# Kernel optimization log

Measured on AMD Instinct MI355X. Metric: run time of the kernel, lower is better.

Reference implementation:

```python
import jax, jax.numpy as jnp
import numpy as np

B, C, H = 8, 512, 2048
GROUPS = 32
EPS = 1e-6


def setup_inputs() -> dict:
    key = jax.random.key(0)
    ks = jax.random.split(key, 10)
    s = 1.0 / np.sqrt(C)
    return {
        "x": jax.random.normal(ks[0], (B, C, H), dtype=jnp.float32),
        "gamma": jnp.ones((C,), jnp.float32),
        "beta": jnp.zeros((C,), jnp.float32),
        "wq": jax.random.normal(ks[1], (C, C), jnp.float32) * s,
        "bq": jnp.zeros((C,), jnp.float32),
        "wk": jax.random.normal(ks[2], (C, C), jnp.float32) * s,
        "bk": jnp.zeros((C,), jnp.float32),
        "wv": jax.random.normal(ks[3], (C, C), jnp.float32) * s,
        "bv": jnp.zeros((C,), jnp.float32),
        "wp": jax.random.normal(ks[4], (C, C), jnp.float32) * s,
        "bp": jnp.zeros((C,), jnp.float32),
    }


def group_norm(x, gamma, beta):
    b, c, h = x.shape
    xr = x.reshape(b, GROUPS, c // GROUPS, h)
    mean = xr.mean(axis=(2, 3), keepdims=True)
    var = xr.var(axis=(2, 3), keepdims=True)
    xn = ((xr - mean) * jax.lax.rsqrt(var + EPS)).reshape(b, c, h)
    return xn * gamma[None, :, None] + beta[None, :, None]


def conv1x1(x, w, b):
    # 1x1 Conv1d == channel-mixing GEMM: [C_out,C_in] x [b,C_in,h]
    return jnp.einsum("oc,bch->boh", w, x) + b[None, :, None]


def reference(x, gamma, beta, wq, bq, wk, bk, wv, bv, wp, bp):
    b, c, h = x.shape
    hn = group_norm(x, gamma, beta)
    q = conv1x1(hn, wq, bq)  # [b,c,h]
    k = conv1x1(hn, wk, bk)
    v = conv1x1(hn, wv, bv)
    # scores w[b,i,j] = sum_c q[b,c,i] k[b,c,j] / sqrt(c)
    w = jnp.einsum("bci,bcj->bij", q, k) * (c ** -0.5)
    w = jax.nn.softmax(w, axis=2)
    # h_[b,c,i] = sum_j v[b,c,j] w[b,i,j]
    h_ = jnp.einsum("bcj,bij->bci", v, w)
    out = conv1x1(h_, wp, bp)
    return x + out
```

## Files before the change

### kernel.cpp

```cpp
#include <hip/hip_runtime.h>
#include <stdint.h>

typedef unsigned short u16;
typedef short s16x8 __attribute__((ext_vector_type(8)));
typedef float f32x4 __attribute__((ext_vector_type(4)));

#define BM 128
#define BN 128
#define BK 32
#define KPAD 40

__device__ __forceinline__ float bf2f(u16 b) {
    union { unsigned int u; float f; } v; v.u = ((unsigned int)b) << 16; return v.f;
}
__device__ __forceinline__ u16 f2bf(float f) {
    union { float f; unsigned int u; } v; v.f = f;
    unsigned int u = v.u;
    u += 0x7fffu + ((u >> 16) & 1u);
    return (u16)(u >> 16);
}
__device__ __forceinline__ void async_cp16(const u16* g, u16* l) {
    __builtin_amdgcn_global_load_lds((const __attribute__((address_space(1))) void*)g,
                                     (__attribute__((address_space(3))) void*)l, 16, 0, 0);
}

__global__ __launch_bounds__(256) void gn_stats(const float* __restrict__ x,
                                                float* __restrict__ mean,
                                                float* __restrict__ rstd) {
    const int bg = blockIdx.x;
    const float* p = x + (long)bg * 16 * 2048;
    float s = 0.f, ss = 0.f;
    for (int it = 0; it < 32; it++) {
        const float4 v = *reinterpret_cast<const float4*>(p + ((it * 256 + threadIdx.x) << 2));
        s += v.x + v.y + v.z + v.w;
        ss += v.x * v.x + v.y * v.y + v.z * v.z + v.w * v.w;
    }
    const int lane = threadIdx.x & 63, wave = threadIdx.x >> 6;
#pragma unroll
    for (int o = 32; o > 0; o >>= 1) { s += __shfl_down(s, o, 64); ss += __shfl_down(ss, o, 64); }
    __shared__ float rb[8];
    if (lane == 0) { rb[wave] = s; rb[4 + wave] = ss; }
    __syncthreads();
    if (threadIdx.x == 0) {
        float S = rb[0] + rb[1] + rb[2] + rb[3];
        float SS = rb[4] + rb[5] + rb[6] + rb[7];
        float mu = S * (1.f / 32768.f);
        float var = SS * (1.f / 32768.f) - mu * mu;
        mean[bg] = mu;
        rstd[bg] = rsqrtf(var + 1e-6f);
    }
}

__global__ __launch_bounds__(256) void gn_apply_t(const float* __restrict__ x,
                                                  const float* __restrict__ gamma,
                                                  const float* __restrict__ beta,
                                                  const float* __restrict__ mean,
                                                  const float* __restrict__ rstd,
                                                  u16* __restrict__ hnT) {
    const int b = blockIdx.z, c0 = blockIdx.y * 64, h0 = blockIdx.x * 64;
    __shared__ __align__(16) u16 T[64][72];
    const int tid = threadIdx.x;
#pragma unroll
    for (int sidx = 0; sidx < 4; sidx++) {
        int ch = tid + sidx * 256;
        int cc = ch >> 4, h4 = (ch & 15) * 4;
        int c = c0 + cc;
        float mu = mean[b * 32 + (c >> 4)], rs = rstd[b * 32 + (c >> 4)];
        float ga = gamma[c], be = beta[c];
        const float4 v = *reinterpret_cast<const float4*>(x + ((long)b * 512 + c) * 2048 + h0 + h4);
        ushort4 pk;
        pk.x = f2bf((v.x - mu) * rs * ga + be);
        pk.y = f2bf((v.y - mu) * rs * ga + be);
        pk.z = f2bf((v.z - mu) * rs * ga + be);
        pk.w = f2bf((v.w - mu) * rs * ga + be);
        *reinterpret_cast<ushort4*>(&T[cc][h4]) = pk;
    }
    __syncthreads();
#pragma unroll
    for (int sidx = 0; sidx < 2; sidx++) {
        int ch = tid + sidx * 256;
        int hh = ch >> 3, c8 = (ch & 7) * 8;
        unsigned int o[4];
#pragma unroll
        for (int i = 0; i < 4; i++) {
            u16 lo = T[c8 + 2 * i][hh];
            u16 hi = T[c8 + 2 * i + 1][hh];
            o[i] = (unsigned int)lo | ((unsigned int)hi << 16);
        }
        *reinterpret_cast<uint4*>(hnT + ((long)b * 2048 + h0 + hh) * 512 + c0 + c8) =
            uint4{o[0], o[1], o[2], o[3]};
    }
}

__global__ __launch_bounds__(256) void w2bf(const float* __restrict__ a,
                                            const float* __restrict__ b,
                                            const float* __restrict__ c,
                                            u16* __restrict__ dst) {
    const float* s = (blockIdx.y == 0) ? a : (blockIdx.y == 1) ? b : c;
    const int i = (blockIdx.x * 256 + threadIdx.x) * 4;
    const float4 v = *reinterpret_cast<const float4*>(s + i);
    ushort4 p;
    p.x = f2bf(v.x); p.y = f2bf(v.y); p.z = f2bf(v.z); p.w = f2bf(v.w);
    *reinterpret_cast<ushort4*>(dst + (long)blockIdx.y * 262144 + i) = p;
}

__global__ __launch_bounds__(256) void softmax_rows(u16* __restrict__ S) {
    u16* p = S + (long)blockIdx.x * 2048;
    const int tid = threadIdx.x;
    uint4 v = *reinterpret_cast<const uint4*>(p + (tid << 3));
    unsigned int w[4] = {v.x, v.y, v.z, v.w};
    float f[8];
#pragma unroll
    for (int i = 0; i < 4; i++) {
        f[2 * i]     = bf2f((u16)(w[i] & 0xffffu));
        f[2 * i + 1] = bf2f((u16)(w[i] >> 16));
    }
    float m = f[0];
#pragma unroll
    for (int i = 1; i < 8; i++) m = fmaxf(m, f[i]);
    const int lane = tid & 63, wave = tid >> 6;
#pragma unroll
    for (int o = 32; o > 0; o >>= 1) m = fmaxf(m, __shfl_down(m, o, 64));
    __shared__ float rb[4];
    __shared__ float bc;
    if (lane == 0) rb[wave] = m;
    __syncthreads();
    if (tid == 0) bc = fmaxf(fmaxf(rb[0], rb[1]), fmaxf(rb[2], rb[3]));
    __syncthreads();
    m = bc;
    float s = 0.f;
#pragma unroll
    for (int i = 0; i < 8; i++) { f[i] = __expf(f[i] - m); s += f[i]; }
#pragma unroll
    for (int o = 32; o > 0; o >>= 1) s += __shfl_down(s, o, 64);
    __syncthreads();
    if (lane == 0) rb[wave] = s;
    __syncthreads();
    if (tid == 0) bc = 1.f / (rb[0] + rb[1] + rb[2] + rb[3]);
    __syncthreads();
    const float inv = bc;
#pragma unroll
    for (int i = 0; i < 4; i++)
        w[i] = (unsigned int)f2bf(f[2 * i] * inv) | ((unsigned int)f2bf(f[2 * i + 1] * inv) << 16);
    *reinterpret_cast<uint4*>(p + (tid << 3)) = uint4{w[0], w[1], w[2], w[3]};
}

template <int EPI>
__global__ __launch_bounds__(256) void gemm_tn_a(const u16* __restrict__ Ag, long sA,
                                                 const u16* __restrict__ Bg, long sB,
                                                 const float* __restrict__ bias,
                                                 const float* __restrict__ Xg, long sX,
                                                 void* __restrict__ Ogv, long sO,
                                                 int K, int lda, int ldb, int ldo,
                                                 float scale) {
    const int b = blockIdx.z;
    Ag += (long)b * sA;
    Bg += (long)b * sB;
    const int m0 = blockIdx.y * BM;
    const int n0 = blockIdx.x * BN;

    __shared__ __align__(16) u16 As[BM * BK];
    __shared__ __align__(16) u16 Bs[BN * BK];

    const int tid = threadIdx.x;
    const int wave = tid >> 6;
    const int lane = tid & 63;
    const int quad = lane >> 4;
    const int l16 = lane & 15;
    const int wm = (wave >> 1) * 64;
    const int wn = (wave & 1) * 64;
    const int rl = lane >> 2;
    const int cl = (lane & 3) * 8;

    f32x4 acc[4][4];
#pragma unroll
    for (int i = 0; i < 4; i++)
#pragma unroll
        for (int j = 0; j < 4; j++) acc[i][j] = f32x4{0.f, 0.f, 0.f, 0.f};

    for (int k0 = 0; k0 < K; k0 += BK) {
        __syncthreads();
#pragma unroll
        for (int j = 0; j < 2; j++) {
            const int rbase = wave * 32 + j * 16;
            async_cp16(Ag + (long)(m0 + rbase + rl) * lda + k0 + cl, &As[rbase * BK]);
            async_cp16(Bg + (long)(n0 + rbase + rl) * ldb + k0 + cl, &Bs[rbase * BK]);
        }
        __syncthreads();
        s16x8 af[4], bfr[4];
#pragma unroll
        for (int i = 0; i < 4; i++)
            af[i] = *reinterpret_cast<const s16x8*>(&As[(wm + i * 16 + l16) * BK + quad * 8]);
#pragma unroll
        for (int j = 0; j < 4; j++)
            bfr[j] = *reinterpret_cast<const s16x8*>(&Bs[(wn + j * 16 + l16) * BK + quad * 8]);
#pragma unroll
        for (int i = 0; i < 4; i++)
#pragma unroll
            for (int j = 0; j < 4; j++)
                acc[i][j] = __builtin_amdgcn_mfma_f32_16x16x32_bf16(af[i], bfr[j], acc[i][j], 0, 0, 0);
    }

#pragma unroll
    for (int i = 0; i < 4; i++) {
        const int mb = m0 + wm + i * 16 + quad * 4;
#pragma unroll
        for (int j = 0; j < 4; j++) {
            const int n = n0 + wn + j * 16 + l16;
            if (EPI == 0) {
                u16* O = (u16*)Ogv + (long)b * sO;
#pragma unroll
                for (int r = 0; r < 4; r++) {
                    float vv = acc[i][j][r] * scale;
                    if (bias) vv += bias[mb + r];
                    O[(long)(mb + r) * ldo + n] = f2bf(vv);
                }
            } else if (EPI == 1) {
                u16* O = (u16*)Ogv + (long)b * sO;
                ushort4 pk;
                pk.x = f2bf(acc[i][j][0] + bias[mb + 0]);
                pk.y = f2bf(acc[i][j][1] + bias[mb + 1]);
                pk.z = f2bf(acc[i][j][2] + bias[mb + 2]);
                pk.w = f2bf(acc[i][j][3] + bias[mb + 3]);
                *reinterpret_cast<ushort4*>(&O[(long)n * ldo + mb]) = pk;
            } else {
                float* O = (float*)Ogv + (long)b * sO;
                const float* X = Xg + (long)b * sX;
                const float bn = bias[n];
                const float4 xv = *reinterpret_cast<const float4*>(&X[(long)n * ldo + mb]);
                float4 pk;
                pk.x = acc[i][j][0] + bn + xv.x;
                pk.y = acc[i][j][1] + bn + xv.y;
                pk.z = acc[i][j][2] + bn + xv.z;
                pk.w = acc[i][j][3] + bn + xv.w;
                *reinterpret_cast<float4*>(&O[(long)n * ldo + mb]) = pk;
            }
        }
    }
}

template <int F32>
__device__ __forceinline__ void stage_tile(const char* G, int ld, int r0, int k0,
                                           u16* __restrict__ lds, int tid) {
    if (F32) {
        const float* g = (const float*)G;
#pragma unroll
        for (int s = 0; s < 4; s++) {
            const int c = tid + s * 256;
            const int row = c >> 3, col = (c & 7) * 4;
            const float4 v = *reinterpret_cast<const float4*>(g + (long)(r0 + row) * ld + k0 + col);
            ushort4 pk;
            pk.x = f2bf(v.x); pk.y = f2bf(v.y); pk.z = f2bf(v.z); pk.w = f2bf(v.w);
            *reinterpret_cast<ushort4*>(&lds[row * KPAD + col]) = pk;
        }
    } else {
        const u16* g = (const u16*)G;
#pragma unroll
        for (int s = 0; s < 2; s++) {
            const int c = tid + s * 256;
            const int row = c >> 2, col = (c & 3) * 8;
            const uint4 v = *reinterpret_cast<const uint4*>(g + (long)(r0 + row) * ld + k0 + col);
            *reinterpret_cast<uint4*>(&lds[row * KPAD + col]) = v;
        }
    }
}

template <int EPI, int AF32, int BF32>
__global__ __launch_bounds__(256) void gemm_tn(const void* __restrict__ Agv, long sA,
                                               const void* __restrict__ Bgv, long sB,
                                               const float* __restrict__ bias,
                                               const float* __restrict__ Xg, long sX,
                                               void* __restrict__ Ogv, long sO,
                                               int K, int lda, int ldb, int ldo,
                                               float scale) {
    const int b = blockIdx.z;
    const char* A8 = (const char*)Agv + (long)b * sA * (AF32 ? 4 : 2);
    const char* B8 = (const char*)Bgv + (long)b * sB * (BF32 ? 4 : 2);
    const int m0 = blockIdx.y * BM;
    const int n0 = blockIdx.x * BN;

    __shared__ __align__(16) u16 As[BM * KPAD];
    __shared__ __align__(16) u16 Bs[BN * KPAD];

    const int tid = threadIdx.x;
    const int wave = tid >> 6;
    const int lane = tid & 63;
    const int quad = lane >> 4;
    const int l16 = lane & 15;
    const int wm = (wave >> 1) * 64;
    const int wn = (wave & 1) * 64;

    f32x4 acc[4][4];
#pragma unroll
    for (int i = 0; i < 4; i++)
#pragma unroll
        for (int j = 0; j < 4; j++) acc[i][j] = f32x4{0.f, 0.f, 0.f, 0.f};

    for (int k0 = 0; k0 < K; k0 += BK) {
        __syncthreads();
        stage_tile<AF32>(A8, lda, m0, k0, As, tid);
        stage_tile<BF32>(B8, ldb, n0, k0, Bs, tid);
        __syncthreads();
        s16x8 af[4], bfr[4];
#pragma unroll
        for (int i = 0; i < 4; i++)
            af[i] = *reinterpret_cast<const s16x8*>(&As[(wm + i * 16 + l16) * KPAD + quad * 8]);
#pragma unroll
        for (int j = 0; j < 4; j++)
            bfr[j] = *reinterpret_cast<const s16x8*>(&Bs[(wn + j * 16 + l16) * KPAD + quad * 8]);
#pragma unroll
        for (int i = 0; i < 4; i++)
#pragma unroll
            for (int j = 0; j < 4; j++)
                acc[i][j] = __builtin_amdgcn_mfma_f32_16x16x32_bf16(af[i], bfr[j], acc[i][j], 0, 0, 0);
    }

#pragma unroll
    for (int i = 0; i < 4; i++) {
        const int mb = m0 + wm + i * 16 + quad * 4;
#pragma unroll
        for (int j = 0; j < 4; j++) {
            const int n = n0 + wn + j * 16 + l16;
            if (EPI == 0) {
                u16* O = (u16*)Ogv + (long)b * sO;
#pragma unroll
                for (int r = 0; r < 4; r++) {
                    float vv = acc[i][j][r] * scale;
                    if (bias) vv += bias[mb + r];
                    O[(long)(mb + r) * ldo + n] = f2bf(vv);
                }
            } else if (EPI == 1) {
                u16* O = (u16*)Ogv + (long)b * sO;
                ushort4 pk;
                pk.x = f2bf(acc[i][j][0] + bias[mb + 0]);
                pk.y = f2bf(acc[i][j][1] + bias[mb + 1]);
                pk.z = f2bf(acc[i][j][2] + bias[mb + 2]);
                pk.w = f2bf(acc[i][j][3] + bias[mb + 3]);
                *reinterpret_cast<ushort4*>(&O[(long)n * ldo + mb]) = pk;
            } else {
                float* O = (float*)Ogv + (long)b * sO;
                const float* X = Xg + (long)b * sX;
                const float bn = bias[n];
                const float4 xv = *reinterpret_cast<const float4*>(&X[(long)n * ldo + mb]);
                float4 pk;
                pk.x = acc[i][j][0] + bn + xv.x;
                pk.y = acc[i][j][1] + bn + xv.y;
                pk.z = acc[i][j][2] + bn + xv.z;
                pk.w = acc[i][j][3] + bn + xv.w;
                *reinterpret_cast<float4*>(&O[(long)n * ldo + mb]) = pk;
            }
        }
    }
}

extern "C" void kernel_launch(void* const* d_in, const int* in_sizes, int n_in,
                              void* d_out, int out_size, void* d_ws, size_t ws_size,
                              hipStream_t stream) {
    const float* x     = (const float*)d_in[0];
    const float* gamma = (const float*)d_in[1];
    const float* beta  = (const float*)d_in[2];
    const float* wq    = (const float*)d_in[3];
    const float* bq    = (const float*)d_in[4];
    const float* wk    = (const float*)d_in[5];
    const float* bk    = (const float*)d_in[6];
    const float* wv    = (const float*)d_in[7];
    const float* bv    = (const float*)d_in[8];
    const float* wp    = (const float*)d_in[9];
    const float* bp    = (const float*)d_in[10];
    float* out = (float*)d_out;

    const long HC = (long)2048 * 512;
    const long HH = (long)2048 * 2048;
    const long WSZ = 512 * 512;
    const float scl = 0.044194173824159216f;

    char* ws = (char*)d_ws;
    float* meanb = (float*)ws;
    float* rstdb = (float*)(ws + 1024);
    u16* base = (u16*)(ws + 4096);

    const size_t FULL_NEED   = 4096 + 2 * (size_t)(24 * HC + 8 * HH);
    const size_t MED_NEED    = 4096 + 2 * (size_t)(32 * HC + HH);
    const size_t SMALL_NEED  = 4096 + 2 * (size_t)(4 * HC + HH);
    const size_t CHUNK512    = 4096 + 2 * (size_t)(4 * HC + 512 * 2048);

    gn_stats<<<256, 256, 0, stream>>>(x, meanb, rstdb);

    if (ws_size >= FULL_NEED) {
        u16* qT  = base;
        u16* kT  = qT + 8 * HC;
        u16* vv  = kT + 8 * HC;
        u16* Sb  = vv + 8 * HC;
        u16* hnT = Sb;
        u16* wb3 = Sb + 8 * HH - 3 * WSZ;
        u16* hT  = qT;
        u16* wpb = vv;

        w2bf<<<dim3(256, 3), 256, 0, stream>>>(wq, wk, wv, wb3);
        gn_apply_t<<<dim3(32, 8, 8), 256, 0, stream>>>(x, gamma, beta, meanb, rstdb, hnT);
        gemm_tn_a<1><<<dim3(16, 4, 8), 256, 0, stream>>>(wb3 + 0 * WSZ, 0, hnT, HC, bq, nullptr, 0,
                                                         qT, HC, 512, 512, 512, 512, 1.f);
        gemm_tn_a<1><<<dim3(16, 4, 8), 256, 0, stream>>>(wb3 + 1 * WSZ, 0, hnT, HC, bk, nullptr, 0,
                                                         kT, HC, 512, 512, 512, 512, 1.f);
        gemm_tn_a<0><<<dim3(16, 4, 8), 256, 0, stream>>>(wb3 + 2 * WSZ, 0, hnT, HC, bv, nullptr, 0,
                                                         vv, HC, 512, 512, 512, 2048, 1.f);
        gemm_tn_a<0><<<dim3(16, 16, 8), 256, 0, stream>>>(qT, HC, kT, HC, nullptr, nullptr, 0,
                                                          Sb, HH, 512, 512, 512, 2048, scl);
        softmax_rows<<<16384, 256, 0, stream>>>(Sb);
        gemm_tn_a<0><<<dim3(4, 16, 8), 256, 0, stream>>>(Sb, HH, vv, HC, nullptr, nullptr, 0,
                                                         hT, HC, 2048, 2048, 2048, 512, 1.f);
        w2bf<<<dim3(256, 1), 256, 0, stream>>>(wp, wp, wp, wpb);
        gemm_tn_a<2><<<dim3(4, 16, 8), 256, 0, stream>>>(hT, HC, wpb, 0, bp, x, HC,
                                                         out, HC, 512, 512, 512, 2048, 1.f);
    } else if (ws_size >= MED_NEED) {
        u16* hnT = base;
        u16* qT  = hnT + 8 * HC;
        u16* kT  = qT + 8 * HC;
        u16* vv  = kT + 8 * HC;
        u16* Sb  = vv + 8 * HC;
        u16* hT  = hnT;
        gn_apply_t<<<dim3(32, 8, 8), 256, 0, stream>>>(x, gamma, beta, meanb, rstdb, hnT);
        gemm_tn<1, 1, 0><<<dim3(16, 4, 8), 256, 0, stream>>>(wq, 0, hnT, HC, bq, nullptr, 0,
                                                             qT, HC, 512, 512, 512, 512, 1.f);
        gemm_tn<1, 1, 0><<<dim3(16, 4, 8), 256, 0, stream>>>(wk, 0, hnT, HC, bk, nullptr, 0,
                                                             kT, HC, 512, 512, 512, 512, 1.f);
        gemm_tn<0, 1, 0><<<dim3(16, 4, 8), 256, 0, stream>>>(wv, 0, hnT, HC, bv, nullptr, 0,
                                                             vv, HC, 512, 512, 512, 2048, 1.f);
        for (int b = 0; b < 8; b++) {
            gemm_tn<0, 0, 0><<<dim3(16, 16, 1), 256, 0, stream>>>(qT + b * HC, 0, kT + b * HC, 0,
                                                                  nullptr, nullptr, 0, Sb, 0,
                                                                  512, 512, 512, 2048, scl);
            softmax_rows<<<2048, 256, 0, stream>>>(Sb);
            gemm_tn<0, 0, 0><<<dim3(4, 16, 1), 256, 0, stream>>>(Sb, 0, vv + b * HC, 0,
                                                                 nullptr, nullptr, 0, hT + b * HC, 0,
                                                                 2048, 2048, 2048, 512, 1.f);
        }
        gemm_tn<2, 0, 1><<<dim3(4, 16, 8), 256, 0, stream>>>(hT, HC, wp, 0, bp, x, HC,
                                                             out, HC, 512, 512, 512, 2048, 1.f);
    } else {
        const int CH = (ws_size >= SMALL_NEED) ? 2048 : ((ws_size >= CHUNK512) ? 512 : 128);
        u16* hn = base;
        u16* q  = hn + HC;
        u16* k  = q + HC;
        u16* v  = k + HC;
        u16* Sc = v + HC;
        u16* hT = hn;
        for (int b = 0; b < 8; b++) {
            const float* xb = x + (long)b * HC;
            gn_apply_t<<<dim3(32, 8, 1), 256, 0, stream>>>(xb, gamma, beta,
                                                           meanb + b * 32, rstdb + b * 32, hn);
            gemm_tn<1, 1, 0><<<dim3(16, 4, 1), 256, 0, stream>>>(wq, 0, hn, 0, bq, nullptr, 0,
                                                                 q, 0, 512, 512, 512, 512, 1.f);
            gemm_tn<1, 1, 0><<<dim3(16, 4, 1), 256, 0, stream>>>(wk, 0, hn, 0, bk, nullptr, 0,
                                                                 k, 0, 512, 512, 512, 512, 1.f);
            gemm_tn<0, 1, 0><<<dim3(16, 4, 1), 256, 0, stream>>>(wv, 0, hn, 0, bv, nullptr, 0,
                                                                 v, 0, 512, 512, 512, 2048, 1.f);
            for (int i0 = 0; i0 < 2048; i0 += CH) {
                gemm_tn<0, 0, 0><<<dim3(16, CH / 128, 1), 256, 0, stream>>>(
                    q + (long)i0 * 512, 0, k, 0, nullptr, nullptr, 0, Sc, 0,
                    512, 512, 512, 2048, scl);
                softmax_rows<<<CH, 256, 0, stream>>>(Sc);
                gemm_tn<0, 0, 0><<<dim3(4, CH / 128, 1), 256, 0, stream>>>(
                    Sc, 0, v, 0, nullptr, nullptr, 0, hT + (long)i0 * 512, 0,
                    2048, 2048, 2048, 512, 1.f);
            }
            gemm_tn<2, 0, 1><<<dim3(4, 16, 1), 256, 0, stream>>>(hT, 0, wp, 0, bp, xb, 0,
                                                                 out + (long)b * HC, 0,
                                                                 512, 512, 512, 2048, 1.f);
        }
    }
}
```

Before: 337.2 us.

## Double-buffer LDS staging in GEMM and fuse QKV projections into one launch

The GEMM main loop now keeps two LDS buffers and issues the async global-to-LDS copy for the next K tile before computing on the current one. This hides load latency and cuts the barriers per K step from two to one. The three separate Q/K/V projection launches are merged into one kernel with a grid of 24 in z, which picks weight, bias and output layout per block. This removes two launches and gives a larger grid, at the cost of doubled LDS per block, which may reduce occupancy.

```diff
diff --git a/kernel.cpp b/kernel.cpp
--- a/kernel.cpp
+++ b/kernel.cpp
@@ -159,8 +159,8 @@
     const int m0 = blockIdx.y * BM;
     const int n0 = blockIdx.x * BN;
 
-    __shared__ __align__(16) u16 As[BM * BK];
-    __shared__ __align__(16) u16 Bs[BN * BK];
+    __shared__ __align__(16) u16 As[2][BM * BK];
+    __shared__ __align__(16) u16 Bs[2][BN * BK];
 
     const int tid = threadIdx.x;
     const int wave = tid >> 6;
@@ -178,27 +178,37 @@
 #pragma unroll
         for (int j = 0; j < 4; j++) acc[i][j] = f32x4{0.f, 0.f, 0.f, 0.f};
 
-    for (int k0 = 0; k0 < K; k0 += BK) {
-        __syncthreads();
+    auto stage = [&](int buf, int k0) {
 #pragma unroll
         for (int j = 0; j < 2; j++) {
             const int rbase = wave * 32 + j * 16;
-            async_cp16(Ag + (long)(m0 + rbase + rl) * lda + k0 + cl, &As[rbase * BK]);
-            async_cp16(Bg + (long)(n0 + rbase + rl) * ldb + k0 + cl, &Bs[rbase * BK]);
-        }
-        __syncthreads();
+            async_cp16(Ag + (long)(m0 + rbase + rl) * lda + k0 + cl, &As[buf][rbase * BK]);
+            async_cp16(Bg + (long)(n0 + rbase + rl) * ldb + k0 + cl, &Bs[buf][rbase * BK]);
+        }
+    };
+    auto compute = [&](int buf) {
         s16x8 af[4], bfr[4];
 #pragma unroll
         for (int i = 0; i < 4; i++)
-            af[i] = *reinterpret_cast<const s16x8*>(&As[(wm + i * 16 + l16) * BK + quad * 8]);
+            af[i] = *reinterpret_cast<const s16x8*>(&As[buf][(wm + i * 16 + l16) * BK + quad * 8]);
 #pragma unroll
         for (int j = 0; j < 4; j++)
-            bfr[j] = *reinterpret_cast<const s16x8*>(&Bs[(wn + j * 16 + l16) * BK + quad * 8]);
+            bfr[j] = *reinterpret_cast<const s16x8*>(&Bs[buf][(wn + j * 16 + l16) * BK + quad * 8]);
 #pragma unroll
         for (int i = 0; i < 4; i++)
 #pragma unroll
             for (int j = 0; j < 4; j++)
                 acc[i][j] = __builtin_amdgcn_mfma_f32_16x16x32_bf16(af[i], bfr[j], acc[i][j], 0, 0, 0);
+    };
+
+    stage(0, 0);
+    for (int k0 = 0; k0 < K; k0 += 2 * BK) {
+        __syncthreads();
+        stage(1, k0 + BK);
+        compute(0);
+        __syncthreads();
+        if (k0 + 2 * BK < K) stage(0, k0 + 2 * BK);
+        compute(1);
     }
 
 #pragma unroll
@@ -239,6 +249,106 @@
     }
 }
 
+__global__ __launch_bounds__(256) void qkv_a(const u16* __restrict__ wb3,
+                                             const u16* __restrict__ hnT,
+                                             const float* __restrict__ bq,
+                                             const float* __restrict__ bk,
+                                             const float* __restrict__ bv,
+                                             u16* __restrict__ qT, u16* __restrict__ kT,
+                                             u16* __restrict__ vv) {
+    const long HC = 1048576;
+    const int z = blockIdx.z;
+    const int which = z % 3, b = z / 3;
+    const u16* Ag = wb3 + which * 262144;
+    const u16* Bg = hnT + (long)b * HC;
+    const int m0 = blockIdx.y * BM;
+    const int n0 = blockIdx.x * BN;
+
+    __shared__ __align__(16) u16 As[2][BM * BK];
+    __shared__ __align__(16) u16 Bs[2][BN * BK];
+
+    const int tid = threadIdx.x;
+    const int wave = tid >> 6;
+    const int lane = tid & 63;
+    const int quad = lane >> 4;
+    const int l16 = lane & 15;
+    const int wm = (wave >> 1) * 64;
+    const int wn = (wave & 1) * 64;
+    const int rl = lane >> 2;
+    const int cl = (lane & 3) * 8;
+
+    f32x4 acc[4][4];
+#pragma unroll
+    for (int i = 0; i < 4; i++)
+#pragma unroll
+        for (int j = 0; j < 4; j++) acc[i][j] = f32x4{0.f, 0.f, 0.f, 0.f};
+
+    auto stage = [&](int buf, int k0) {
+#pragma unroll
+        for (int j = 0; j < 2; j++) {
+            const int rbase = wave * 32 + j * 16;
+            async_cp16(Ag + (long)(m0 + rbase + rl) * 512 + k0 + cl, &As[buf][rbase * BK]);
+            async_cp16(Bg + (long)(n0 + rbase + rl) * 512 + k0 + cl, &Bs[buf][rbase * BK]);
+        }
+    };
+    auto compute = [&](int buf) {
+        s16x8 af[4], bfr[4];
+#pragma unroll
+        for (int i = 0; i < 4; i++)
+            af[i] = *reinterpret_cast<const s16x8*>(&As[buf][(wm + i * 16 + l16) * BK + quad * 8]);
+#pragma unroll
+        for (int j = 0; j < 4; j++)
+            bfr[j] = *reinterpret_cast<const s16x8*>(&Bs[buf][(wn + j * 16 + l16) * BK + quad * 8]);
+#pragma unroll
+        for (int i = 0; i < 4; i++)
+#pragma unroll
+            for (int j = 0; j < 4; j++)
+                acc[i][j] = __builtin_amdgcn_mfma_f32_16x16x32_bf16(af[i], bfr[j], acc[i][j], 0, 0, 0);
+    };
+
+    stage(0, 0);
+    for (int k0 = 0; k0 < 512; k0 += 2 * BK) {
+        __syncthreads();
+        stage(1, k0 + BK);
+        compute(0);
+        __syncthreads();
+        if (k0 + 2 * BK < 512) stage(0, k0 + 2 * BK);
+        compute(1);
+    }
+
+    if (which == 2) {
+        u16* O = vv + (long)b * HC;
+#pragma unroll
+        for (int i = 0; i < 4; i++) {
+            const int mb = m0 + wm + i * 16 + quad * 4;
+#pragma unroll
+            for (int j = 0; j < 4; j++) {
+                const int n = n0 + wn + j * 16 + l16;
+#pragma unroll
+                for (int r = 0; r < 4; r++)
+                    O[(long)(mb + r) * 2048 + n] = f2bf(acc[i][j][r] + bv[mb + r]);
+            }
+        }
+    } else {
+        const float* bias = which ? bk : bq;
+        u16* O = (which ? kT : qT) + (long)b * HC;
+#pragma unroll
+        for (int i = 0; i < 4; i++) {
+            const int mb = m0 + wm + i * 16 + quad * 4;
+#pragma unroll
+            for (int j = 0; j < 4; j++) {
+                const int n = n0 + wn + j * 16 + l16;
+                ushort4 pk;
+                pk.x = f2bf(acc[i][j][0] + bias[mb + 0]);
+                pk.y = f2bf(acc[i][j][1] + bias[mb + 1]);
+                pk.z = f2bf(acc[i][j][2] + bias[mb + 2]);
+                pk.w = f2bf(acc[i][j][3] + bias[mb + 3]);
+                *reinterpret_cast<ushort4*>(&O[(long)n * 512 + mb]) = pk;
+            }
+        }
+    }
+}
+
 template <int F32>
 __device__ __forceinline__ void stage_tile(const char* G, int ld, int r0, int k0,
                                            u16* __restrict__ lds, int tid) {
@@ -398,12 +508,7 @@
 
         w2bf<<<dim3(256, 3), 256, 0, stream>>>(wq, wk, wv, wb3);
         gn_apply_t<<<dim3(32, 8, 8), 256, 0, stream>>>(x, gamma, beta, meanb, rstdb, hnT);
-        gemm_tn_a<1><<<dim3(16, 4, 8), 256, 0, stream>>>(wb3 + 0 * WSZ, 0, hnT, HC, bq, nullptr, 0,
-                                                         qT, HC, 512, 512, 512, 512, 1.f);
-        gemm_tn_a<1><<<dim3(16, 4, 8), 256, 0, stream>>>(wb3 + 1 * WSZ, 0, hnT, HC, bk, nullptr, 0,
-                                                         kT, HC, 512, 512, 512, 512, 1.f);
-        gemm_tn_a<0><<<dim3(16, 4, 8), 256, 0, stream>>>(wb3 + 2 * WSZ, 0, hnT, HC, bv, nullptr, 0,
-                                                         vv, HC, 512, 512, 512, 2048, 1.f);
+        qkv_a<<<dim3(16, 4, 24), 256, 0, stream>>>(wb3, hnT, bq, bk, bv, qT, kT, vv);
         gemm_tn_a<0><<<dim3(16, 16, 8), 256, 0, stream>>>(qT, HC, kT, HC, nullptr, nullptr, 0,
                                                           Sb, HH, 512, 512, 512, 2048, scl);
         softmax_rows<<<16384, 256, 0, stream>>>(Sb);
```

New measurement: 325.3 us. 1.04x faster.
